# Kernel optimization log

Measured on AMD Instinct MI355X. Metric: run time of the kernel, lower is better.

Reference implementation:

```python
import jax, jax.numpy as jnp
import numpy as np

N_USERS = 50000
N_ENTITIES = 100000
N_RELATIONS = 16
N_EDGES = 3200000
NNZ = 2500000
CH = 64
N_HOPS = 2


def l2_normalize(x, eps=1e-12):
    # matches torch F.normalize(dim=1): x / max(||x||_2, eps)
    n = jnp.sqrt(jnp.sum(x * x, axis=-1, keepdims=True))
    return x / jnp.maximum(n, eps)


def setup_inputs() -> dict:
    key = jax.random.key(0)
    ks = jax.random.split(key, 10)
    user_emb = jax.random.normal(ks[0], (N_USERS, CH), dtype=jnp.float32)
    entity_emb = jax.random.normal(ks[1], (N_ENTITIES, CH), dtype=jnp.float32)
    weight = jax.random.normal(ks[2], (N_RELATIONS, CH), dtype=jnp.float32)
    triplet_mask = jax.random.uniform(ks[3], (N_EDGES,), dtype=jnp.float32)
    interact_vals = jnp.ones((NNZ,), dtype=jnp.float32)
    edge_head = jax.random.randint(ks[4], (N_EDGES,), 0, N_ENTITIES, dtype=jnp.int32)
    edge_tail = jax.random.randint(ks[5], (N_EDGES,), 0, N_ENTITIES, dtype=jnp.int32)
    edge_type = jax.random.randint(ks[6], (N_EDGES,), 1, N_RELATIONS + 1, dtype=jnp.int32)
    interact_rows = jax.random.randint(ks[7], (NNZ,), 0, N_USERS, dtype=jnp.int32)
    interact_cols = jax.random.randint(ks[8], (NNZ,), 0, N_ENTITIES, dtype=jnp.int32)
    return {
        'user_emb': user_emb, 'entity_emb': entity_emb, 'weight': weight,
        'triplet_mask': triplet_mask, 'interact_vals': interact_vals,
        'edge_head': edge_head, 'edge_tail': edge_tail, 'edge_type': edge_type,
        'interact_rows': interact_rows, 'interact_cols': interact_cols,
    }


def reference(user_emb, entity_emb, weight, triplet_mask, interact_vals,
              edge_head, edge_tail, edge_type, interact_rows, interact_cols):
    unmask = triplet_mask
    entity_res = entity_emb
    user_res = user_emb
    for _ in range(N_HOPS):
        # KG aggregate: gather tail embeddings, mask + relation multiply, scatter-sum to heads
        neigh = entity_emb[edge_tail] * unmask[:, None] * weight[edge_type - 1]  # [E, CH]
        entity_agg = jax.ops.segment_sum(neigh, edge_head, num_segments=N_ENTITIES)
        # user aggregate: sparse interact_mat @ entity_emb (COO gather + segment_sum)
        user_agg = jax.ops.segment_sum(
            interact_vals[:, None] * entity_emb[interact_cols],
            interact_rows, num_segments=N_USERS)
        # mess_dropout disabled (eval mode -> identity)
        entity_emb = l2_normalize(entity_agg)
        user_emb = l2_normalize(user_agg)
        entity_res = entity_res + entity_emb
        user_res = user_res + user_emb
    return entity_res, user_res
```

## Files before the change

### kernel.cpp

```cpp
#include <hip/hip_runtime.h>

#define N_USERS 50000
#define N_ENTITIES 100000
#define N_RELATIONS 16
#define N_EDGES 3200000
#define NNZ 2500000
#define CH 64

#define RPB 64
#define NB_E 1563
#define NB_U 782
#define NBUCKETS (NB_E + NB_U)
#define STAGE 3840

#define NCE 49
#define NCU 25
#define CAPC_E 67072
#define CAPC_U 104448
#define NCU_DOUT 14

#define PA_KG 256
#define PA_U  192
#define SE 10
#define SU 16

__device__ __forceinline__ unsigned short f2bf(float f) {
    unsigned u = __float_as_uint(f);
    u += 0x7FFF + ((u >> 16) & 1);
    return (unsigned short)(u >> 16);
}

__device__ __forceinline__ int wave_incl_scan(int v, int lane) {
    int s = v;
    #pragma unroll
    for (int d = 1; d < 64; d <<= 1) {
        int x = __shfl_up(s, d, 64);
        if (lane >= d) s += x;
    }
    return s;
}

__global__ void __launch_bounds__(1024)
passA_kernel(const int* __restrict__ head, const int* __restrict__ tail,
             const int* __restrict__ type, const float* __restrict__ maskp,
             const int* __restrict__ irows, const int* __restrict__ icols,
             const float* __restrict__ ivals,
             int* __restrict__ fineCnt, int* __restrict__ cCurE,
             int* __restrict__ cCurU,
             int2* __restrict__ cbE, int2* __restrict__ cbU_d,
             int2* __restrict__ cbU_w) {
    __shared__ int histF[NB_E];
    __shared__ int histC[64];
    __shared__ int lbase[64];
    __shared__ int2* utab[NCU];
    const int blk = blockIdx.x;
    const int t = threadIdx.x;

    if (blk < PA_KG) {
        for (int i = t; i < NB_E; i += 1024) histF[i] = 0;
        if (t < NCE) histC[t] = 0;
        __syncthreads();
        const int chunk = (N_EDGES + PA_KG - 1) / PA_KG;
        int base = blk * chunk, lim = min(base + chunk, N_EDGES);
        for (int i = base + t; i < lim; i += 1024) {
            int h = head[i];
            atomicAdd(&histF[h >> 6], 1);
            atomicAdd(&histC[h >> 11], 1);
        }
        __syncthreads();
        for (int i = t; i < NB_E; i += 1024)
            if (histF[i]) atomicAdd(&fineCnt[NB_U + i], histF[i]);
        if (t < NCE) {
            int c = histC[t];
            lbase[t] = c ? atomicAdd(&cCurE[t], c) : 0;
            histC[t] = 0;
        }
        __syncthreads();
        int i = base + t;
        for (; i + 3072 < lim; i += 4096) {
            int i0 = i, i1 = i + 1024, i2 = i + 2048, i3 = i + 3072;
            int h0 = head[i0], h1 = head[i1], h2 = head[i2], h3 = head[i3];
            int x0 = tail[i0] | ((type[i0] - 1) << 17) | ((h0 & 63) << 21) | (((h0 >> 6) & 31) << 27);
            int x1 = tail[i1] | ((type[i1] - 1) << 17) | ((h1 & 63) << 21) | (((h1 >> 6) & 31) << 27);
            int x2 = tail[i2] | ((type[i2] - 1) << 17) | ((h2 & 63) << 21) | (((h2 >> 6) & 31) << 27);
            int x3 = tail[i3] | ((type[i3] - 1) << 17) | ((h3 & 63) << 21) | (((h3 >> 6) & 31) << 27);
            float m0 = maskp[i0], m1 = maskp[i1], m2 = maskp[i2], m3 = maskp[i3];
            int c0 = h0 >> 11, c1 = h1 >> 11, c2 = h2 >> 11, c3 = h3 >> 11;
            int l0 = lbase[c0] + atomicAdd(&histC[c0], 1);
            int l1 = lbase[c1] + atomicAdd(&histC[c1], 1);
            int l2 = lbase[c2] + atomicAdd(&histC[c2], 1);
            int l3 = lbase[c3] + atomicAdd(&histC[c3], 1);
            if (l0 < CAPC_E) cbE[(size_t)c0 * CAPC_E + l0] = make_int2(x0, __float_as_int(m0));
            if (l1 < CAPC_E) cbE[(size_t)c1 * CAPC_E + l1] = make_int2(x1, __float_as_int(m1));
            if (l2 < CAPC_E) cbE[(size_t)c2 * CAPC_E + l2] = make_int2(x2, __float_as_int(m2));
            if (l3 < CAPC_E) cbE[(size_t)c3 * CAPC_E + l3] = make_int2(x3, __float_as_int(m3));
        }
        for (; i < lim; i += 1024) {
            int h = head[i];
            int x = tail[i] | ((type[i] - 1) << 17) | ((h & 63) << 21) | (((h >> 6) & 31) << 27);
            int c = h >> 11;
            int loc = lbase[c] + atomicAdd(&histC[c], 1);
            if (loc < CAPC_E)
                cbE[(size_t)c * CAPC_E + loc] = make_int2(x, __float_as_int(maskp[i]));
        }
    } else {
        if (t < NCU)
            utab[t] = (t < NCU_DOUT) ? (cbU_d + (size_t)t * CAPC_U)
                                     : (cbU_w + (size_t)(t - NCU_DOUT) * CAPC_U);
        for (int i = t; i < NB_U; i += 1024) histF[i] = 0;
        if (t < NCU) histC[t] = 0;
        __syncthreads();
        const int ub = blk - PA_KG;
        const int chunk = (NNZ + PA_U - 1) / PA_U;
        int base = ub * chunk, lim = min(base + chunk, NNZ);
        for (int i = base + t; i < lim; i += 1024) {
            int r = irows[i];
            atomicAdd(&histF[r >> 6], 1);
            atomicAdd(&histC[r >> 11], 1);
        }
        __syncthreads();
        for (int i = t; i < NB_U; i += 1024)
            if (histF[i]) atomicAdd(&fineCnt[i], histF[i]);
        if (t < NCU) {
            int c = histC[t];
            lbase[t] = c ? atomicAdd(&cCurU[t], c) : 0;
            histC[t] = 0;
        }
        __syncthreads();
        int i = base + t;
        for (; i + 3072 < lim; i += 4096) {
            int i0 = i, i1 = i + 1024, i2 = i + 2048, i3 = i + 3072;
            int r0 = irows[i0], r1 = irows[i1], r2 = irows[i2], r3 = irows[i3];
            int x0 = icols[i0] | ((r0 & 63) << 17) | (((r0 >> 6) & 31) << 27);
            int x1 = icols[i1] | ((r1 & 63) << 17) | (((r1 >> 6) & 31) << 27);
            int x2 = icols[i2] | ((r2 & 63) << 17) | (((r2 >> 6) & 31) << 27);
            int x3 = icols[i3] | ((r3 & 63) << 17) | (((r3 >> 6) & 31) << 27);
            float v0 = ivals[i0], v1 = ivals[i1], v2 = ivals[i2], v3 = ivals[i3];
            int c0 = r0 >> 11, c1 = r1 >> 11, c2 = r2 >> 11, c3 = r3 >> 11;
            int l0 = lbase[c0] + atomicAdd(&histC[c0], 1);
            int l1 = lbase[c1] + atomicAdd(&histC[c1], 1);
            int l2 = lbase[c2] + atomicAdd(&histC[c2], 1);
            int l3 = lbase[c3] + atomicAdd(&histC[c3], 1);
            if (l0 < CAPC_U) utab[c0][l0] = make_int2(x0, __float_as_int(v0));
            if (l1 < CAPC_U) utab[c1][l1] = make_int2(x1, __float_as_int(v1));
            if (l2 < CAPC_U) utab[c2][l2] = make_int2(x2, __float_as_int(v2));
            if (l3 < CAPC_U) utab[c3][l3] = make_int2(x3, __float_as_int(v3));
        }
        for (; i < lim; i += 1024) {
            int r = irows[i];
            int x = icols[i] | ((r & 63) << 17) | (((r >> 6) & 31) << 27);
            int c = r >> 11;
            int loc = lbase[c] + atomicAdd(&histC[c], 1);
            if (loc < CAPC_U) utab[c][loc] = make_int2(x, __float_as_int(ivals[i]));
        }
    }
}

__global__ void __launch_bounds__(512)
scan_kernel(const int* __restrict__ fineCnt, int* __restrict__ fineBase,
            int* __restrict__ fineCur) {
    __shared__ int wsums[8];
    __shared__ int carry_s;
    const int t = threadIdx.x, w = t >> 6, lane = t & 63;
    if (t == 0) carry_s = 0;
    __syncthreads();
    for (int base = 0; base < NBUCKETS; base += 512) {
        int i = base + t;
        int v = (i < NBUCKETS) ? fineCnt[i] : 0;
        int s = wave_incl_scan(v, lane);
        if (lane == 63) wsums[w] = s;
        __syncthreads();
        int carry = carry_s;
        if (w == 0) {
            int ws = (lane < 8) ? wsums[lane] : 0;
            int ss = wave_incl_scan(ws, lane);
            if (lane < 8) wsums[lane] = ss - ws;
        }
        __syncthreads();
        int excl = s - v + wsums[w] + carry;
        if (i < NBUCKETS) { fineBase[i] = excl; fineCur[i] = excl; }
        __syncthreads();
        if (t == 511) carry_s = excl + v;
        __syncthreads();
    }
}

__global__ void __launch_bounds__(1024)
passB_kernel(const int* __restrict__ cCurE, const int* __restrict__ cCurU,
             const int2* __restrict__ cbE, const int2* __restrict__ cbU_d,
             const int2* __restrict__ cbU_w,
             int* __restrict__ fineCur, int2* __restrict__ binAll) {
    __shared__ int h32[32];
    __shared__ int lb[32];
    const int blk = blockIdx.x, t = threadIdx.x;
    const int2* __restrict__ src;
    int cnt, sub, S, fid0;
    if (blk < NCE * SE) {
        int c = blk / SE; sub = blk % SE; S = SE;
        cnt = min(cCurE[c], CAPC_E);
        src = cbE + (size_t)c * CAPC_E;
        fid0 = NB_U + c * 32;
    } else {
        int c = (blk - NCE * SE) / SU; sub = (blk - NCE * SE) % SU; S = SU;
        cnt = min(cCurU[c], CAPC_U);
        src = (c < NCU_DOUT) ? cbU_d + (size_t)c * CAPC_U
                             : cbU_w + (size_t)(c - NCU_DOUT) * CAPC_U;
        fid0 = c * 32;
    }
    int len = (cnt + S - 1) / S;
    int b0 = sub * len, b1 = min(b0 + len, cnt);
    if (t < 32) h32[t] = 0;
    __syncthreads();
    for (int i = b0 + t; i < b1; i += 1024)
        atomicAdd(&h32[(src[i].x >> 27) & 31], 1);
    __syncthreads();
    if (t < 32) {
        int c2 = h32[t];
        lb[t] = c2 ? atomicAdd(&fineCur[fid0 + t], c2) : 0;
        h32[t] = 0;
    }
    __syncthreads();
    int i = b0 + t;
    for (; i + 3072 < b1; i += 4096) {
        int2 e0 = src[i], e1 = src[i + 1024], e2 = src[i + 2048], e3 = src[i + 3072];
        int f0 = (e0.x >> 27) & 31, f1 = (e1.x >> 27) & 31;
        int f2 = (e2.x >> 27) & 31, f3 = (e3.x >> 27) & 31;
        int l0 = lb[f0] + atomicAdd(&h32[f0], 1);
        int l1 = lb[f1] + atomicAdd(&h32[f1], 1);
        int l2 = lb[f2] + atomicAdd(&h32[f2], 1);
        int l3 = lb[f3] + atomicAdd(&h32[f3], 1);
        binAll[l0] = e0; binAll[l1] = e1; binAll[l2] = e2; binAll[l3] = e3;
    }
    for (; i < b1; i += 1024) {
        int2 e = src[i];
        int f = (e.x >> 27) & 31;
        binAll[lb[f] + atomicAdd(&h32[f], 1)] = e;
    }
}

__global__ void __launch_bounds__(512)
sortinit_kernel(int2* __restrict__ binAll, const int* __restrict__ fineCnt,
                const int* __restrict__ fineBase, int* __restrict__ rowptr,
                const float4* __restrict__ user_emb,
                const float4* __restrict__ entity_emb,
                ushort4* __restrict__ cur_bf,
                float4* __restrict__ out_entity, float4* __restrict__ out_user) {
    __shared__ int2 buf[STAGE];
    __shared__ int2 sbuf[STAGE];
    __shared__ int  hist[RPB];
    __shared__ int  offs[RPB + 1];

    const int blk = blockIdx.x;
    const int t = threadIdx.x;
    if (blk >= NBUCKETS) {
        const int ne4 = N_ENTITIES * CH / 4;
        const int nu4 = N_USERS * CH / 4;
        int i = (blk - NBUCKETS) * 512 + t;
        if (i < ne4) {
            float4 v = entity_emb[i];
            out_entity[i] = v;
            ushort4 bq;
            bq.x = f2bf(v.x); bq.y = f2bf(v.y); bq.z = f2bf(v.z); bq.w = f2bf(v.w);
            cur_bf[i] = bq;
        }
        if (i < nu4) out_user[i] = user_emb[i];
        return;
    }

    const int b = blk;
    const bool is_user = (b < NB_U);
    const int base = fineBase[b];
    int2* __restrict__ bin = binAll + base;
    const int cnt = min(fineCnt[b], STAGE);
    const int rsh = is_user ? 17 : 21;

    if (t < RPB) hist[t] = 0;
    for (int i = t; i < cnt; i += 512) buf[i] = bin[i];
    __syncthreads();
    for (int i = t; i < cnt; i += 512)
        atomicAdd(&hist[(buf[i].x >> rsh) & 63], 1);
    __syncthreads();
    if (t < 64) {
        int v = hist[t];
        int s = wave_incl_scan(v, t);
        offs[t] = s - v;
        if (t == 63) offs[64] = s;
    }
    __syncthreads();
    if (t < RPB) hist[t] = 0;
    __syncthreads();
    for (int i = t; i < cnt; i += 512) {
        int2 p = buf[i];
        int r = (p.x >> rsh) & 63;
        int k = atomicAdd(&hist[r], 1);
        sbuf[offs[r] + k] = p;
    }
    __syncthreads();
    for (int i = t; i < cnt; i += 512) bin[i] = sbuf[i];
    if (t <= 64) rowptr[b * 65 + t] = base + offs[t];
}

__global__ void __launch_bounds__(512)
agg_kernel(const uint2* __restrict__ cur64,
           const float* __restrict__ weight,
           const int2* __restrict__ binAll, const int* __restrict__ rowptr,
           unsigned short* __restrict__ nxt,
           float* __restrict__ res_e, float* __restrict__ res_u) {
    __shared__ float4 wl4[N_RELATIONS * 16];
    __shared__ int    srp[RPB + 1];

    const int b = blockIdx.x;
    const int t = threadIdx.x;
    const int w = t >> 6;
    const int lane = t & 63;
    const int g = lane >> 4;
    const int c2 = lane & 15;
    const bool is_user = (b < NB_U);
    const int eb = b - NB_U;

    if (!is_user)
        for (int i = t; i < N_RELATIONS * 16; i += 512)
            wl4[i] = ((const float4*)weight)[i];
    if (t < RPB + 1) srp[t] = rowptr[b * 65 + t];
    __syncthreads();

    #pragma unroll
    for (int rr = 0; rr < 8; ++rr) {
        const int row = (w << 3) + rr;
        const int s = srp[row], e = srp[row + 1];
        float x0 = 0.f, x1 = 0.f, x2 = 0.f, x3 = 0.f;
        int i = s;
        if (is_user) {
            for (; i + 7 < e; i += 8) {
                int2 pa = binAll[i + g];
                int2 pb = binAll[i + 4 + g];
                uint2 qa = cur64[(size_t)(pa.x & 0x1FFFF) * 16 + c2];
                uint2 qb = cur64[(size_t)(pb.x & 0x1FFFF) * 16 + c2];
                float sa = __int_as_float(pa.y);
                float sb = __int_as_float(pb.y);
                x0 += __uint_as_float(qa.x << 16) * sa;
                x1 += __uint_as_float(qa.x & 0xFFFF0000u) * sa;
                x2 += __uint_as_float(qa.y << 16) * sa;
                x3 += __uint_as_float(qa.y & 0xFFFF0000u) * sa;
                x0 += __uint_as_float(qb.x << 16) * sb;
                x1 += __uint_as_float(qb.x & 0xFFFF0000u) * sb;
                x2 += __uint_as_float(qb.y << 16) * sb;
                x3 += __uint_as_float(qb.y & 0xFFFF0000u) * sb;
            }
            for (; i < e; i += 4) {
                int idx = i + g;
                bool vld = idx < e;
                int2 p = binAll[vld ? idx : i];
                uint2 q = cur64[(size_t)(p.x & 0x1FFFF) * 16 + c2];
                float sv = vld ? __int_as_float(p.y) : 0.f;
                x0 += __uint_as_float(q.x << 16) * sv;
                x1 += __uint_as_float(q.x & 0xFFFF0000u) * sv;
                x2 += __uint_as_float(q.y << 16) * sv;
                x3 += __uint_as_float(q.y & 0xFFFF0000u) * sv;
            }
        } else {
            for (; i + 7 < e; i += 8) {
                int2 pa = binAll[i + g];
                int2 pb = binAll[i + 4 + g];
                uint2 qa = cur64[(size_t)(pa.x & 0x1FFFF) * 16 + c2];
                uint2 qb = cur64[(size_t)(pb.x & 0x1FFFF) * 16 + c2];
                float4 wa = wl4[((pa.x >> 17) & 15) * 16 + c2];
                float4 wb = wl4[((pb.x >> 17) & 15) * 16 + c2];
                float sa = __int_as_float(pa.y);
                float sb = __int_as_float(pb.y);
                x0 += __uint_as_float(qa.x << 16) * (sa * wa.x);
                x1 += __uint_as_float(qa.x & 0xFFFF0000u) * (sa * wa.y);
                x2 += __uint_as_float(qa.y << 16) * (sa * wa.z);
                x3 += __uint_as_float(qa.y & 0xFFFF0000u) * (sa * wa.w);
                x0 += __uint_as_float(qb.x << 16) * (sb * wb.x);
                x1 += __uint_as_float(qb.x & 0xFFFF0000u) * (sb * wb.y);
                x2 += __uint_as_float(qb.y << 16) * (sb * wb.z);
                x3 += __uint_as_float(qb.y & 0xFFFF0000u) * (sb * wb.w);
            }
            for (; i < e; i += 4) {
                int idx = i + g;
                bool vld = idx < e;
                int2 p = binAll[vld ? idx : i];
                uint2 q = cur64[(size_t)(p.x & 0x1FFFF) * 16 + c2];
                float4 wv = wl4[((p.x >> 17) & 15) * 16 + c2];
                float sv = vld ? __int_as_float(p.y) : 0.f;
                x0 += __uint_as_float(q.x << 16) * (sv * wv.x);
                x1 += __uint_as_float(q.x & 0xFFFF0000u) * (sv * wv.y);
                x2 += __uint_as_float(q.y << 16) * (sv * wv.z);
                x3 += __uint_as_float(q.y & 0xFFFF0000u) * (sv * wv.w);
            }
        }

        x0 += __shfl_xor(x0, 16, 64); x0 += __shfl_xor(x0, 32, 64);
        x1 += __shfl_xor(x1, 16, 64); x1 += __shfl_xor(x1, 32, 64);
        x2 += __shfl_xor(x2, 16, 64); x2 += __shfl_xor(x2, 32, 64);
        x3 += __shfl_xor(x3, 16, 64); x3 += __shfl_xor(x3, 32, 64);
        float ss = x0 * x0 + x1 * x1 + x2 * x2 + x3 * x3;
        #pragma unroll
        for (int o = 8; o; o >>= 1) ss += __shfl_xor(ss, o, 64);
        float inv = 1.f / fmaxf(sqrtf(ss), 1e-12f);
        float y0 = x0 * inv, y1 = x1 * inv, y2 = x2 * inv, y3 = x3 * inv;
        if (g == 0) {
            if (is_user) {
                int grow = b * RPB + row;
                if (grow < N_USERS) {
                    float4* p = (float4*)res_u + (size_t)grow * 16 + c2;
                    float4 v = *p;
                    v.x += y0; v.y += y1; v.z += y2; v.w += y3;
                    *p = v;
                }
            } else {
                int grow = eb * RPB + row;
                if (grow < N_ENTITIES) {
                    uint2 pk;
                    pk.x = (unsigned)f2bf(y0) | ((unsigned)f2bf(y1) << 16);
                    pk.y = (unsigned)f2bf(y2) | ((unsigned)f2bf(y3) << 16);
                    ((uint2*)nxt)[(size_t)grow * 16 + c2] = pk;
                    float4* p = (float4*)res_e + (size_t)grow * 16 + c2;
                    float4 v = *p;
                    v.x += y0; v.y += y1; v.z += y2; v.w += y3;
                    *p = v;
                }
            }
        }
    }
}

extern "C" void kernel_launch(void* const* d_in, const int* in_sizes, int n_in,
                              void* d_out, int out_size, void* d_ws, size_t ws_size,
                              hipStream_t stream) {
    const float* user_emb   = (const float*)d_in[0];
    const float* entity_emb = (const float*)d_in[1];
    const float* weight     = (const float*)d_in[2];
    const float* mask       = (const float*)d_in[3];
    const float* ivals      = (const float*)d_in[4];
    const int*   edge_head  = (const int*)d_in[5];
    const int*   edge_tail  = (const int*)d_in[6];
    const int*   edge_type  = (const int*)d_in[7];
    const int*   irows      = (const int*)d_in[8];
    const int*   icols      = (const int*)d_in[9];

    float* out_entity = (float*)d_out;
    float* out_user   = (float*)d_out + (size_t)N_ENTITIES * CH;

    int2* cbE   = (int2*)d_out;
    int2* cbU_d = cbE + (size_t)NCE * CAPC_E;

    unsigned short* curA = (unsigned short*)d_ws;
    unsigned short* curB = curA + (size_t)N_ENTITIES * CH;
    int2* binAll = (int2*)(curB + (size_t)N_ENTITIES * CH);
    int2* cbU_w  = binAll + (size_t)(N_EDGES + NNZ);
    int*  fineCnt  = (int*)(cbU_w + (size_t)(NCU - NCU_DOUT) * CAPC_U);
    int*  cCurE    = fineCnt + NBUCKETS;
    int*  cCurU    = cCurE + NCE;
    int*  fineBase = cCurU + NCU;
    int*  fineCur  = fineBase + NBUCKETS;
    int*  rowptr   = fineCur + NBUCKETS;

    hipMemsetAsync(fineCnt, 0, (size_t)(NBUCKETS + NCE + NCU) * sizeof(int), stream);

    passA_kernel<<<PA_KG + PA_U, 1024, 0, stream>>>(
        edge_head, edge_tail, edge_type, mask, irows, icols, ivals,
        fineCnt, cCurE, cCurU, cbE, cbU_d, cbU_w);

    scan_kernel<<<1, 512, 0, stream>>>(fineCnt, fineBase, fineCur);

    passB_kernel<<<NCE * SE + NCU * SU, 1024, 0, stream>>>(
        cCurE, cCurU, cbE, cbU_d, cbU_w, fineCur, binAll);

    {
        const int init_blocks = (N_ENTITIES * CH / 4 + 511) / 512;
        sortinit_kernel<<<NBUCKETS + init_blocks, 512, 0, stream>>>(
            binAll, fineCnt, fineBase, rowptr,
            (const float4*)user_emb, (const float4*)entity_emb,
            (ushort4*)curA, (float4*)out_entity, (float4*)out_user);
    }

    agg_kernel<<<NBUCKETS, 512, 0, stream>>>(
        (const uint2*)curA, weight, binAll, rowptr,
        curB, out_entity, out_user);
    agg_kernel<<<NBUCKETS, 512, 0, stream>>>(
        (const uint2*)curB, weight, binAll, rowptr,
        curA, out_entity, out_user);
}
```

Measured before the change: 522.1 us.

## Replace bucket sort plus local row sort with per-row counting sort

Pass A now counts edges per destination row with global atomics instead of per-64-row bucket histograms. A three-kernel hierarchical scan then builds per-row offsets, and pass B scatters each entry straight to its final row position, so the separate shared-memory sortinit pass is gone. The bf16 packing of entity embeddings moves into extra blocks of pass A. The residual copy is dropped: the first aggregation reads the original embeddings as its residual source. The cost is contended global atomics on about 150K row counters and scattered writes to binAll.

```diff
diff --git a/kernel.cpp b/kernel.cpp
--- a/kernel.cpp
+++ b/kernel.cpp
@@ -11,7 +11,8 @@
 #define NB_E 1563
 #define NB_U 782
 #define NBUCKETS (NB_E + NB_U)
-#define STAGE 3840
+#define NROWS_U (NB_U * 64)
+#define NROWS_PAD (NBUCKETS * 64)
 
 #define NCE 49
 #define NCU 25
@@ -21,6 +22,7 @@
 
 #define PA_KG 256
 #define PA_U  192
+#define PACK_BLOCKS 1563
 #define SE 10
 #define SU 16
 
@@ -45,31 +47,40 @@
              const int* __restrict__ type, const float* __restrict__ maskp,
              const int* __restrict__ irows, const int* __restrict__ icols,
              const float* __restrict__ ivals,
-             int* __restrict__ fineCnt, int* __restrict__ cCurE,
+             const float4* __restrict__ entity_emb, ushort4* __restrict__ cur_bf,
+             int* __restrict__ rowCnt, int* __restrict__ cCurE,
              int* __restrict__ cCurU,
              int2* __restrict__ cbE, int2* __restrict__ cbU_d,
              int2* __restrict__ cbU_w) {
-    __shared__ int histF[NB_E];
     __shared__ int histC[64];
     __shared__ int lbase[64];
     __shared__ int2* utab[NCU];
     const int blk = blockIdx.x;
     const int t = threadIdx.x;
 
+    if (blk >= PA_KG + PA_U) {
+        const int ne4 = N_ENTITIES * CH / 4;
+        int i = (blk - PA_KG - PA_U) * 1024 + t;
+        if (i < ne4) {
+            float4 v = entity_emb[i];
+            ushort4 bq;
+            bq.x = f2bf(v.x); bq.y = f2bf(v.y); bq.z = f2bf(v.z); bq.w = f2bf(v.w);
+            cur_bf[i] = bq;
+        }
+        return;
+    }
+
     if (blk < PA_KG) {
-        for (int i = t; i < NB_E; i += 1024) histF[i] = 0;
         if (t < NCE) histC[t] = 0;
         __syncthreads();
         const int chunk = (N_EDGES + PA_KG - 1) / PA_KG;
         int base = blk * chunk, lim = min(base + chunk, N_EDGES);
         for (int i = base + t; i < lim; i += 1024) {
             int h = head[i];
-            atomicAdd(&histF[h >> 6], 1);
+            atomicAdd(&rowCnt[NROWS_U + h], 1);
             atomicAdd(&histC[h >> 11], 1);
         }
         __syncthreads();
-        for (int i = t; i < NB_E; i += 1024)
-            if (histF[i]) atomicAdd(&fineCnt[NB_U + i], histF[i]);
         if (t < NCE) {
             int c = histC[t];
             lbase[t] = c ? atomicAdd(&cCurE[t], c) : 0;
@@ -104,23 +115,21 @@
                 cbE[(size_t)c * CAPC_E + loc] = make_int2(x, __float_as_int(maskp[i]));
         }
     } else {
-        if (t < NCU)
+        if (t < NCU) {
             utab[t] = (t < NCU_DOUT) ? (cbU_d + (size_t)t * CAPC_U)
                                      : (cbU_w + (size_t)(t - NCU_DOUT) * CAPC_U);
-        for (int i = t; i < NB_U; i += 1024) histF[i] = 0;
-        if (t < NCU) histC[t] = 0;
+            histC[t] = 0;
+        }
         __syncthreads();
         const int ub = blk - PA_KG;
         const int chunk = (NNZ + PA_U - 1) / PA_U;
         int base = ub * chunk, lim = min(base + chunk, NNZ);
         for (int i = base + t; i < lim; i += 1024) {
             int r = irows[i];
-            atomicAdd(&histF[r >> 6], 1);
+            atomicAdd(&rowCnt[r], 1);
             atomicAdd(&histC[r >> 11], 1);
         }
         __syncthreads();
-        for (int i = t; i < NB_U; i += 1024)
-            if (histF[i]) atomicAdd(&fineCnt[i], histF[i]);
         if (t < NCU) {
             int c = histC[t];
             lbase[t] = c ? atomicAdd(&cCurU[t], c) : 0;
@@ -156,9 +165,19 @@
     }
 }
 
+__global__ void __launch_bounds__(256)
+bscan1_kernel(const int* __restrict__ cnt, int* __restrict__ bsum) {
+    int g = blockIdx.x * 4 + (threadIdx.x >> 6);
+    int lane = threadIdx.x & 63;
+    if (g >= NBUCKETS) return;
+    int v = cnt[g * 64 + lane];
+    #pragma unroll
+    for (int o = 32; o; o >>= 1) v += __shfl_xor(v, o, 64);
+    if (lane == 0) bsum[g] = v;
+}
+
 __global__ void __launch_bounds__(512)
-scan_kernel(const int* __restrict__ fineCnt, int* __restrict__ fineBase,
-            int* __restrict__ fineCur) {
+bscan2_kernel(const int* __restrict__ bsum, int* __restrict__ bbase) {
     __shared__ int wsums[8];
     __shared__ int carry_s;
     const int t = threadIdx.x, w = t >> 6, lane = t & 63;
@@ -166,7 +185,7 @@
     __syncthreads();
     for (int base = 0; base < NBUCKETS; base += 512) {
         int i = base + t;
-        int v = (i < NBUCKETS) ? fineCnt[i] : 0;
+        int v = (i < NBUCKETS) ? bsum[i] : 0;
         int s = wave_incl_scan(v, lane);
         if (lane == 63) wsums[w] = s;
         __syncthreads();
@@ -178,133 +197,75 @@
         }
         __syncthreads();
         int excl = s - v + wsums[w] + carry;
-        if (i < NBUCKETS) { fineBase[i] = excl; fineCur[i] = excl; }
+        if (i < NBUCKETS) bbase[i] = excl;
         __syncthreads();
         if (t == 511) carry_s = excl + v;
         __syncthreads();
     }
+}
+
+__global__ void __launch_bounds__(256)
+bscan3_kernel(int* __restrict__ cnt, const int* __restrict__ bbase,
+              int* __restrict__ rowBase) {
+    int g = blockIdx.x * 4 + (threadIdx.x >> 6);
+    int lane = threadIdx.x & 63;
+    if (g >= NBUCKETS) return;
+    int v = cnt[g * 64 + lane];
+    int s = wave_incl_scan(v, lane);
+    int e = bbase[g] + s - v;
+    rowBase[g * 64 + lane] = e;
+    cnt[g * 64 + lane] = e;
+    if (g == NBUCKETS - 1 && lane == 63) rowBase[NROWS_PAD] = e + v;
 }
 
 __global__ void __launch_bounds__(1024)
 passB_kernel(const int* __restrict__ cCurE, const int* __restrict__ cCurU,
              const int2* __restrict__ cbE, const int2* __restrict__ cbU_d,
              const int2* __restrict__ cbU_w,
-             int* __restrict__ fineCur, int2* __restrict__ binAll) {
-    __shared__ int h32[32];
-    __shared__ int lb[32];
+             int* __restrict__ rowCur, int2* __restrict__ binAll) {
     const int blk = blockIdx.x, t = threadIdx.x;
     const int2* __restrict__ src;
-    int cnt, sub, S, fid0;
+    int cnt, sub, S, rbase, rsh;
     if (blk < NCE * SE) {
         int c = blk / SE; sub = blk % SE; S = SE;
         cnt = min(cCurE[c], CAPC_E);
         src = cbE + (size_t)c * CAPC_E;
-        fid0 = NB_U + c * 32;
+        rbase = NROWS_U + c * 2048; rsh = 21;
     } else {
         int c = (blk - NCE * SE) / SU; sub = (blk - NCE * SE) % SU; S = SU;
         cnt = min(cCurU[c], CAPC_U);
         src = (c < NCU_DOUT) ? cbU_d + (size_t)c * CAPC_U
                              : cbU_w + (size_t)(c - NCU_DOUT) * CAPC_U;
-        fid0 = c * 32;
+        rbase = c * 2048; rsh = 17;
     }
     int len = (cnt + S - 1) / S;
     int b0 = sub * len, b1 = min(b0 + len, cnt);
-    if (t < 32) h32[t] = 0;
-    __syncthreads();
-    for (int i = b0 + t; i < b1; i += 1024)
-        atomicAdd(&h32[(src[i].x >> 27) & 31], 1);
-    __syncthreads();
-    if (t < 32) {
-        int c2 = h32[t];
-        lb[t] = c2 ? atomicAdd(&fineCur[fid0 + t], c2) : 0;
-        h32[t] = 0;
-    }
-    __syncthreads();
     int i = b0 + t;
     for (; i + 3072 < b1; i += 4096) {
         int2 e0 = src[i], e1 = src[i + 1024], e2 = src[i + 2048], e3 = src[i + 3072];
-        int f0 = (e0.x >> 27) & 31, f1 = (e1.x >> 27) & 31;
-        int f2 = (e2.x >> 27) & 31, f3 = (e3.x >> 27) & 31;
-        int l0 = lb[f0] + atomicAdd(&h32[f0], 1);
-        int l1 = lb[f1] + atomicAdd(&h32[f1], 1);
-        int l2 = lb[f2] + atomicAdd(&h32[f2], 1);
-        int l3 = lb[f3] + atomicAdd(&h32[f3], 1);
-        binAll[l0] = e0; binAll[l1] = e1; binAll[l2] = e2; binAll[l3] = e3;
+        int r0 = rbase + (((e0.x >> 27) & 31) << 6) + ((e0.x >> rsh) & 63);
+        int r1 = rbase + (((e1.x >> 27) & 31) << 6) + ((e1.x >> rsh) & 63);
+        int r2 = rbase + (((e2.x >> 27) & 31) << 6) + ((e2.x >> rsh) & 63);
+        int r3 = rbase + (((e3.x >> 27) & 31) << 6) + ((e3.x >> rsh) & 63);
+        int p0 = atomicAdd(&rowCur[r0], 1);
+        int p1 = atomicAdd(&rowCur[r1], 1);
+        int p2 = atomicAdd(&rowCur[r2], 1);
+        int p3 = atomicAdd(&rowCur[r3], 1);
+        binAll[p0] = e0; binAll[p1] = e1; binAll[p2] = e2; binAll[p3] = e3;
     }
     for (; i < b1; i += 1024) {
         int2 e = src[i];
-        int f = (e.x >> 27) & 31;
-        binAll[lb[f] + atomicAdd(&h32[f], 1)] = e;
-    }
-}
-
-__global__ void __launch_bounds__(512)
-sortinit_kernel(int2* __restrict__ binAll, const int* __restrict__ fineCnt,
-                const int* __restrict__ fineBase, int* __restrict__ rowptr,
-                const float4* __restrict__ user_emb,
-                const float4* __restrict__ entity_emb,
-                ushort4* __restrict__ cur_bf,
-                float4* __restrict__ out_entity, float4* __restrict__ out_user) {
-    __shared__ int2 buf[STAGE];
-    __shared__ int2 sbuf[STAGE];
-    __shared__ int  hist[RPB];
-    __shared__ int  offs[RPB + 1];
-
-    const int blk = blockIdx.x;
-    const int t = threadIdx.x;
-    if (blk >= NBUCKETS) {
-        const int ne4 = N_ENTITIES * CH / 4;
-        const int nu4 = N_USERS * CH / 4;
-        int i = (blk - NBUCKETS) * 512 + t;
-        if (i < ne4) {
-            float4 v = entity_emb[i];
-            out_entity[i] = v;
-            ushort4 bq;
-            bq.x = f2bf(v.x); bq.y = f2bf(v.y); bq.z = f2bf(v.z); bq.w = f2bf(v.w);
-            cur_bf[i] = bq;
-        }
-        if (i < nu4) out_user[i] = user_emb[i];
-        return;
-    }
-
-    const int b = blk;
-    const bool is_user = (b < NB_U);
-    const int base = fineBase[b];
-    int2* __restrict__ bin = binAll + base;
-    const int cnt = min(fineCnt[b], STAGE);
-    const int rsh = is_user ? 17 : 21;
-
-    if (t < RPB) hist[t] = 0;
-    for (int i = t; i < cnt; i += 512) buf[i] = bin[i];
-    __syncthreads();
-    for (int i = t; i < cnt; i += 512)
-        atomicAdd(&hist[(buf[i].x >> rsh) & 63], 1);
-    __syncthreads();
-    if (t < 64) {
-        int v = hist[t];
-        int s = wave_incl_scan(v, t);
-        offs[t] = s - v;
-        if (t == 63) offs[64] = s;
-    }
-    __syncthreads();
-    if (t < RPB) hist[t] = 0;
-    __syncthreads();
-    for (int i = t; i < cnt; i += 512) {
-        int2 p = buf[i];
-        int r = (p.x >> rsh) & 63;
-        int k = atomicAdd(&hist[r], 1);
-        sbuf[offs[r] + k] = p;
-    }
-    __syncthreads();
-    for (int i = t; i < cnt; i += 512) bin[i] = sbuf[i];
-    if (t <= 64) rowptr[b * 65 + t] = base + offs[t];
+        int r = rbase + (((e.x >> 27) & 31) << 6) + ((e.x >> rsh) & 63);
+        binAll[atomicAdd(&rowCur[r], 1)] = e;
+    }
 }
 
 __global__ void __launch_bounds__(512)
 agg_kernel(const uint2* __restrict__ cur64,
            const float* __restrict__ weight,
-           const int2* __restrict__ binAll, const int* __restrict__ rowptr,
+           const int2* __restrict__ binAll, const int* __restrict__ rowBase,
            unsigned short* __restrict__ nxt,
+           const float4* __restrict__ src_e, const float4* __restrict__ src_u,
            float* __restrict__ res_e, float* __restrict__ res_u) {
     __shared__ float4 wl4[N_RELATIONS * 16];
     __shared__ int    srp[RPB + 1];
@@ -317,11 +278,12 @@
     const int c2 = lane & 15;
     const bool is_user = (b < NB_U);
     const int eb = b - NB_U;
+    const int ro0 = is_user ? b * 64 : NROWS_U + eb * 64;
 
     if (!is_user)
         for (int i = t; i < N_RELATIONS * 16; i += 512)
             wl4[i] = ((const float4*)weight)[i];
-    if (t < RPB + 1) srp[t] = rowptr[b * 65 + t];
+    if (t < RPB + 1) srp[t] = rowBase[ro0 + t];
     __syncthreads();
 
     #pragma unroll
@@ -404,10 +366,9 @@
             if (is_user) {
                 int grow = b * RPB + row;
                 if (grow < N_USERS) {
-                    float4* p = (float4*)res_u + (size_t)grow * 16 + c2;
-                    float4 v = *p;
+                    float4 v = src_u[(size_t)grow * 16 + c2];
                     v.x += y0; v.y += y1; v.z += y2; v.w += y3;
-                    *p = v;
+                    ((float4*)res_u)[(size_t)grow * 16 + c2] = v;
                 }
             } else {
                 int grow = eb * RPB + row;
@@ -416,10 +377,9 @@
                     pk.x = (unsigned)f2bf(y0) | ((unsigned)f2bf(y1) << 16);
                     pk.y = (unsigned)f2bf(y2) | ((unsigned)f2bf(y3) << 16);
                     ((uint2*)nxt)[(size_t)grow * 16 + c2] = pk;
-                    float4* p = (float4*)res_e + (size_t)grow * 16 + c2;
-                    float4 v = *p;
+                    float4 v = src_e[(size_t)grow * 16 + c2];
                     v.x += y0; v.y += y1; v.z += y2; v.w += y3;
-                    *p = v;
+                    ((float4*)res_e)[(size_t)grow * 16 + c2] = v;
                 }
             }
         }
@@ -450,36 +410,33 @@
     unsigned short* curB = curA + (size_t)N_ENTITIES * CH;
     int2* binAll = (int2*)(curB + (size_t)N_ENTITIES * CH);
     int2* cbU_w  = binAll + (size_t)(N_EDGES + NNZ);
-    int*  fineCnt  = (int*)(cbU_w + (size_t)(NCU - NCU_DOUT) * CAPC_U);
-    int*  cCurE    = fineCnt + NBUCKETS;
-    int*  cCurU    = cCurE + NCE;
-    int*  fineBase = cCurU + NCU;
-    int*  fineCur  = fineBase + NBUCKETS;
-    int*  rowptr   = fineCur + NBUCKETS;
-
-    hipMemsetAsync(fineCnt, 0, (size_t)(NBUCKETS + NCE + NCU) * sizeof(int), stream);
-
-    passA_kernel<<<PA_KG + PA_U, 1024, 0, stream>>>(
+    int*  rowCnt  = (int*)(cbU_w + (size_t)(NCU - NCU_DOUT) * CAPC_U);
+    int*  cCurE   = rowCnt + NROWS_PAD;
+    int*  cCurU   = cCurE + NCE;
+    int*  rowBase = cCurU + NCU;
+    int*  bsum    = rowBase + NROWS_PAD + 1;
+    int*  bbase   = bsum + NBUCKETS;
+
+    hipMemsetAsync(rowCnt, 0, (size_t)(NROWS_PAD + NCE + NCU) * sizeof(int), stream);
+
+    passA_kernel<<<PA_KG + PA_U + PACK_BLOCKS, 1024, 0, stream>>>(
         edge_head, edge_tail, edge_type, mask, irows, icols, ivals,
-        fineCnt, cCurE, cCurU, cbE, cbU_d, cbU_w);
-
-    scan_kernel<<<1, 512, 0, stream>>>(fineCnt, fineBase, fineCur);
+        (const float4*)entity_emb, (ushort4*)curA,
+        rowCnt, cCurE, cCurU, cbE, cbU_d, cbU_w);
+
+    bscan1_kernel<<<(NBUCKETS + 3) / 4, 256, 0, stream>>>(rowCnt, bsum);
+    bscan2_kernel<<<1, 512, 0, stream>>>(bsum, bbase);
+    bscan3_kernel<<<(NBUCKETS + 3) / 4, 256, 0, stream>>>(rowCnt, bbase, rowBase);
 
     passB_kernel<<<NCE * SE + NCU * SU, 1024, 0, stream>>>(
-        cCurE, cCurU, cbE, cbU_d, cbU_w, fineCur, binAll);
-
-    {
-        const int init_blocks = (N_ENTITIES * CH / 4 + 511) / 512;
-        sortinit_kernel<<<NBUCKETS + init_blocks, 512, 0, stream>>>(
-            binAll, fineCnt, fineBase, rowptr,
-            (const float4*)user_emb, (const float4*)entity_emb,
-            (ushort4*)curA, (float4*)out_entity, (float4*)out_user);
-    }
+        cCurE, cCurU, cbE, cbU_d, cbU_w, rowCnt, binAll);
 
     agg_kernel<<<NBUCKETS, 512, 0, stream>>>(
-        (const uint2*)curA, weight, binAll, rowptr,
-        curB, out_entity, out_user);
+        (const uint2*)curA, weight, binAll, rowBase, curB,
+        (const float4*)entity_emb, (const float4*)user_emb,
+        out_entity, out_user);
     agg_kernel<<<NBUCKETS, 512, 0, stream>>>(
-        (const uint2*)curB, weight, binAll, rowptr,
-        curA, out_entity, out_user);
-}
+        (const uint2*)curB, weight, binAll, rowBase, curA,
+        (const float4*)out_entity, (const float4*)out_user,
+        out_entity, out_user);
+}
```

Measured after the change: 1.013 ms. 94.1% more time.
